# Kernel optimization log

Hardware: AMD Instinct MI355X
Metric: run time of the kernel (lower is better)

The kernel has to match this reference:

```python
import jax, jax.numpy as jnp
import numpy as np

B, N, C = 4, 2048, 768
H = 12
HD = C // H

def setup_inputs() -> dict:
    key = jax.random.key(0)
    k1, k2, k3, k4, k5 = jax.random.split(key, 5)
    x = jax.random.normal(k1, (B, N, C), dtype=jnp.float32)
    qkv_w = jax.random.normal(k2, (3 * C, C), dtype=jnp.float32) * (1.0 / np.sqrt(C))
    qkv_b = jax.random.normal(k3, (3 * C,), dtype=jnp.float32) * 0.02
    proj_w = jax.random.normal(k4, (C, C), dtype=jnp.float32) * (1.0 / np.sqrt(C))
    proj_b = jax.random.normal(k5, (C,), dtype=jnp.float32) * 0.02
    return {"x": x, "qkv_w": qkv_w, "qkv_b": qkv_b, "proj_w": proj_w, "proj_b": proj_b}

def reference(x, qkv_w, qkv_b, proj_w, proj_b):
    scale = HD ** (-0.5)
    # qkv projection: (B,N,3C)
    qkv = x @ qkv_w.T + qkv_b
    qkv = qkv.reshape(B, N, 3, H, HD).transpose(2, 0, 3, 1, 4)  # (3,B,H,N,HD)
    q, k, v = qkv[0], qkv[1], qkv[2]
    attn = jnp.einsum('bhqd,bhkd->bhqk', q, k) * scale  # (B,H,N,N)
    mask_value = -jnp.finfo(attn.dtype).max
    causal_mask = jnp.triu(jnp.ones((N, N), dtype=bool), k=1)
    attn = jnp.where(causal_mask, mask_value, attn)
    attn = jax.nn.softmax(attn, axis=-1)
    out = jnp.einsum('bhqk,bhkd->bhqd', attn, v)  # (B,H,N,HD)
    out = out.transpose(0, 2, 1, 3).reshape(B, N, C)
    return out @ proj_w.T + proj_b
```

## Files before the change

kernel.cpp:

```cpp
#include <hip/hip_runtime.h>
#include <hip/hip_bf16.h>


typedef __attribute__((ext_vector_type(8))) short bf16x8;
typedef __attribute__((ext_vector_type(4))) float f32x4;
typedef __attribute__((ext_vector_type(16))) float f32x16;

typedef __attribute__((address_space(3))) unsigned int lds_uint;
typedef __attribute__((address_space(1))) const unsigned int gbl_uint;

__device__ __forceinline__ void gload16(const void* g, void* l) {
  __builtin_amdgcn_global_load_lds((gbl_uint*)g, (lds_uint*)l, 16, 0, 0);
}

__device__ __forceinline__ unsigned short f2bf(float f) {
  unsigned u = __float_as_uint(f);
  unsigned rounding = 0x7FFFu + ((u >> 16) & 1u);
  return (unsigned short)((u + rounding) >> 16);
}

__device__ __forceinline__ unsigned cvtpk(float lo, float hi) {
  unsigned r;
  asm("v_cvt_pk_bf16_f32 %0, %1, %2" : "=v"(r) : "v"(lo), "v"(hi));
  return r;
}

__device__ __forceinline__ float exp2a(float x) {
  float r;
  asm("v_exp_f32 %0, %1" : "=v"(r) : "v"(x));
  return r;
}

__global__ void cast_f32_to_bf16(const float* __restrict__ in,
                                 unsigned short* __restrict__ out, int n) {
  int idx = blockIdx.x * blockDim.x + threadIdx.x;
  int stride = gridDim.x * blockDim.x;
  for (int i = idx * 4; i < n; i += stride * 4) {
    float4 v = *reinterpret_cast<const float4*>(in + i);
    ushort4 o;
    o.x = f2bf(v.x); o.y = f2bf(v.y); o.z = f2bf(v.z); o.w = f2bf(v.w);
    *reinterpret_cast<ushort4*>(out + i) = o;
  }
}

template <bool OUT_F32>
__global__ __launch_bounds__(256) void gemm_bt_kernel(
    const unsigned short* __restrict__ A,
    const unsigned short* __restrict__ Bw,
    const float* __restrict__ bias,
    void* __restrict__ Cout,
    int M, int Ncols, int K, int ldc) {
  __shared__ __align__(16) short As[2][4096];
  __shared__ __align__(16) short Bs[2][4096];

  const int t = threadIdx.x;
  const int lane = t & 63;
  const int wave = t >> 6;
  const int wm = wave >> 1;
  const int wn = wave & 1;
  const int m0 = blockIdx.y * 128;
  const int n0 = blockIdx.x * 128;
  const int lrow = lane & 15;
  const int lk = (lane >> 4) * 8;

  const int srow = t >> 2, scol = (t & 3) * 8;
  const unsigned short* gA0 = A + (size_t)(m0 + srow) * K + scol;
  const unsigned short* gA1 = gA0 + (size_t)64 * K;
  const unsigned short* gB0 = Bw + (size_t)(n0 + srow) * K + scol;
  const unsigned short* gB1 = gB0 + (size_t)64 * K;
  const int db0 = wave * 512, db1 = 2048 + wave * 512;

  f32x4 acc[4][4] = {};
  const int nk = K / 32;

  gload16(gA0, &As[0][db0]); gload16(gA1, &As[0][db1]);
  gload16(gB0, &Bs[0][db0]); gload16(gB1, &Bs[0][db1]);

  int cur = 0;
  for (int kk = 0; kk < nk; ++kk) {
    __syncthreads();
    if (kk + 1 < nk) {
      const int off = (kk + 1) * 32;
      gload16(gA0 + off, &As[cur ^ 1][db0]); gload16(gA1 + off, &As[cur ^ 1][db1]);
      gload16(gB0 + off, &Bs[cur ^ 1][db0]); gload16(gB1 + off, &Bs[cur ^ 1][db1]);
    }
    bf16x8 a[4], b[4];
#pragma unroll
    for (int m = 0; m < 4; ++m)
      a[m] = *reinterpret_cast<const bf16x8*>(&As[cur][(wm * 64 + m * 16 + lrow) * 32 + lk]);
#pragma unroll
    for (int n = 0; n < 4; ++n)
      b[n] = *reinterpret_cast<const bf16x8*>(&Bs[cur][(wn * 64 + n * 16 + lrow) * 32 + lk]);
#pragma unroll
    for (int m = 0; m < 4; ++m)
#pragma unroll
      for (int n = 0; n < 4; ++n)
        acc[m][n] = __builtin_amdgcn_mfma_f32_16x16x32_bf16(a[m], b[n], acc[m][n], 0, 0, 0);
    cur ^= 1;
  }

  const int orow0 = (lane >> 4) * 4;
  const int ocol = lane & 15;
#pragma unroll
  for (int m = 0; m < 4; ++m) {
#pragma unroll
    for (int n = 0; n < 4; ++n) {
      const int c = n0 + wn * 64 + n * 16 + ocol;
      const float bv = bias[c];
#pragma unroll
      for (int r = 0; r < 4; ++r) {
        const int rr = m0 + wm * 64 + m * 16 + orow0 + r;
        const float v = acc[m][n][r] + bv;
        if (OUT_F32)
          reinterpret_cast<float*>(Cout)[(size_t)rr * ldc + c] = v;
        else
          reinterpret_cast<unsigned short*>(Cout)[(size_t)rr * ldc + c] = f2bf(v);
      }
    }
  }
}

#define ATT_N 2048
#define ATT_H 12
#define QKV_LD 2304

__global__ __launch_bounds__(256) void transpose_v(
    const unsigned short* __restrict__ qkv, unsigned short* __restrict__ vt) {
  __shared__ __align__(16) short L[128 * 72];
  const int kb = blockIdx.x;
  const int bh = blockIdx.y;
  const int t = threadIdx.x;
  const int b = bh / ATT_H, h = bh % ATT_H;
  const int d0 = (t & 7) * 8;
  const int kl0 = t >> 3;
  const unsigned short* src =
      qkv + (size_t)(b * ATT_N + kb * 128) * QKV_LD + 1536 + h * 64 + d0;
#pragma unroll
  for (int r = 0; r < 4; ++r) {
    const int kl = kl0 + r * 32;
    bf16x8 v = *reinterpret_cast<const bf16x8*>(src + (size_t)kl * QKV_LD);
    *reinterpret_cast<bf16x8*>(&L[kl * 72 + d0]) = v;
  }
  __syncthreads();
  const int d = t >> 2;
  const int c = t & 3;
  unsigned short* dst = vt + (size_t)bh * 64 * ATT_N + (size_t)d * ATT_N + kb * 128;
#pragma unroll
  for (int cc = 0; cc < 4; ++cc) {
    const int kc = cc * 32 + c * 8;
    union { unsigned short s[8]; bf16x8 v; } U;
#pragma unroll
    for (int j = 0; j < 8; ++j) U.s[j] = (unsigned short)L[(kc + j) * 72 + d];
    *reinterpret_cast<bf16x8*>(dst + kc) = U.v;
  }
}

__global__ __launch_bounds__(256) void attn_kernel(
    const unsigned short* __restrict__ qkv,
    const unsigned short* __restrict__ vt,
    unsigned short* __restrict__ out) {
  __shared__ __align__(16) short Ks[2][4096];
  __shared__ __align__(16) short Vs[2][4096];

  const int t = threadIdx.x;
  const int lane = t & 63;
  const int w = t >> 6;
  const int hi = lane >> 5;
  const int l31 = lane & 31;

  const int wid = blockIdx.x;
  const int qb = 15 - (wid / 48);
  const int bh = wid % 48;
  const int b = bh / ATT_H;
  const int h = bh % ATT_H;

  const size_t rowbase = (size_t)b * ATT_N;
  const unsigned short* qptr = qkv + rowbase * QKV_LD + h * 64;
  const unsigned short* kptr = qptr + 768;
  const unsigned short* vtptr = vt + (size_t)bh * 64 * ATT_N;

  const int q0w = qb * 128 + w * 32;
  const int qg = q0w + l31;
  const int nt = (qb + 1) * 2;

  bf16x8 qf[4];
#pragma unroll
  for (int dk = 0; dk < 4; ++dk)
    qf[dk] = *reinterpret_cast<const bf16x8*>(
        qptr + (size_t)(q0w + l31) * QKV_LD + dk * 16 + hi * 8);

  f32x16 O0 = {}, O1 = {};
  float lrun = 0.f;

  int kKr[2], kKc[2];
#pragma unroll
  for (int c = 0; c < 2; ++c) {
    const int i = t + c * 256;
    const int f = i >> 6, ls = i & 63;
    kKr[c] = (f >> 2) * 32 + (ls & 31);
    kKc[c] = (f & 3) * 2 + (ls >> 5);
  }
  const unsigned short* gK0 = kptr + (size_t)kKr[0] * QKV_LD + kKc[0] * 8;
  const unsigned short* gK1 = kptr + (size_t)kKr[1] * QKV_LD + kKc[1] * 8;
  const unsigned short* gV0 = vtptr + (size_t)kKr[0] * ATT_N + kKc[0] * 8;
  const unsigned short* gV1 = vtptr + (size_t)kKr[1] * ATT_N + kKc[1] * 8;
  const int db0 = w * 512, db1 = 2048 + w * 512;

  gload16(gK0, &Ks[0][db0]); gload16(gK1, &Ks[0][db1]);
  gload16(gV0, &Vs[0][db0]); gload16(gV1, &Vs[0][db1]);

  int cur = 0;
  for (int kt = 0; kt < nt; ++kt) {
    const int k0 = kt * 64;
    __syncthreads();
    if (kt + 1 < nt) {
      const size_t advk = (size_t)(k0 + 64) * QKV_LD;
      gload16(gK0 + advk, &Ks[cur ^ 1][db0]); gload16(gK1 + advk, &Ks[cur ^ 1][db1]);
      gload16(gV0 + (k0 + 64), &Vs[cur ^ 1][db0]);
      gload16(gV1 + (k0 + 64), &Vs[cur ^ 1][db1]);
    }

    if (k0 <= q0w + 31) {
      f32x16 S0 = {}, S1 = {};
      __builtin_amdgcn_s_setprio(1);
#pragma unroll
      for (int dk = 0; dk < 4; ++dk) {
        bf16x8 kf = *reinterpret_cast<const bf16x8*>(&Ks[cur][(dk * 64 + lane) * 8]);
        S0 = __builtin_amdgcn_mfma_f32_32x32x16_bf16(kf, qf[dk], S0, 0, 0, 0);
      }
#pragma unroll
      for (int dk = 0; dk < 4; ++dk) {
        bf16x8 kf = *reinterpret_cast<const bf16x8*>(&Ks[cur][((4 + dk) * 64 + lane) * 8]);
        S1 = __builtin_amdgcn_mfma_f32_32x32x16_bf16(kf, qf[dk], S1, 0, 0, 0);
      }
      __builtin_amdgcn_s_setprio(0);

      const float scale2 = 0.18033688f;
      float p0[16], p1[16];
      if (k0 + 63 <= q0w) {
#pragma unroll
        for (int r = 0; r < 16; ++r) {
          p0[r] = exp2a(S0[r] * scale2);
          p1[r] = exp2a(S1[r] * scale2);
        }
      } else {
#pragma unroll
        for (int r = 0; r < 16; ++r) {
          int row = (r & 3) + 8 * (r >> 2) + 4 * hi;
          float e0 = (k0 + row > qg) ? -1e30f : S0[r] * scale2;
          float e1 = (k0 + 32 + row > qg) ? -1e30f : S1[r] * scale2;
          p0[r] = exp2a(e0);
          p1[r] = exp2a(e1);
        }
      }

      float sa = 0.f, sb = 0.f;
#pragma unroll
      for (int r = 0; r < 16; r += 2) { sa += p0[r] + p1[r]; sb += p0[r + 1] + p1[r + 1]; }
      float rsum = sa + sb;
      rsum += __shfl_xor(rsum, 32);
      lrun += rsum;

      bf16x8 Ub[4];
#pragma unroll
      for (int s = 0; s < 2; ++s) {
        unsigned pu[4][2];
#pragma unroll
        for (int m = 0; m < 4; ++m)
#pragma unroll
          for (int c = 0; c < 2; ++c)
            pu[m][c] = s ? cvtpk(p1[4 * m + 2 * c], p1[4 * m + 2 * c + 1])
                         : cvtpk(p0[4 * m + 2 * c], p0[4 * m + 2 * c + 1]);
#pragma unroll
        for (int tt = 0; tt < 2; ++tt) {
          unsigned s0v = hi ? pu[2 * tt][0] : pu[2 * tt + 1][0];
          unsigned s1v = hi ? pu[2 * tt][1] : pu[2 * tt + 1][1];
          unsigned r0 = __shfl_xor(s0v, 32);
          unsigned r1 = __shfl_xor(s1v, 32);
          union { unsigned u[4]; bf16x8 v; } U;
          U.u[0] = hi ? r0 : pu[2 * tt][0];
          U.u[1] = hi ? r1 : pu[2 * tt][1];
          U.u[2] = hi ? pu[2 * tt + 1][0] : r0;
          U.u[3] = hi ? pu[2 * tt + 1][1] : r1;
          Ub[s * 2 + tt] = U.v;
        }
      }

      __builtin_amdgcn_s_setprio(1);
#pragma unroll
      for (int ks = 0; ks < 4; ++ks) {
        bf16x8 vf0 = *reinterpret_cast<const bf16x8*>(&Vs[cur][(ks * 64 + lane) * 8]);
        O0 = __builtin_amdgcn_mfma_f32_32x32x16_bf16(vf0, Ub[ks], O0, 0, 0, 0);
        bf16x8 vf1 = *reinterpret_cast<const bf16x8*>(&Vs[cur][((4 + ks) * 64 + lane) * 8]);
        O1 = __builtin_amdgcn_mfma_f32_32x32x16_bf16(vf1, Ub[ks], O1, 0, 0, 0);
      }
      __builtin_amdgcn_s_setprio(0);
    }
    cur ^= 1;
  }

  const float inv = 1.0f / lrun;
  unsigned short* orow = out + (rowbase + q0w + l31) * 768 + h * 64;
#pragma unroll
  for (int half = 0; half < 2; ++half) {
    const f32x16& O = half ? O1 : O0;
#pragma unroll
    for (int m = 0; m < 4; ++m) {
      uint2 o2;
      o2.x = cvtpk(O[4 * m + 0] * inv, O[4 * m + 1] * inv);
      o2.y = cvtpk(O[4 * m + 2] * inv, O[4 * m + 3] * inv);
      *reinterpret_cast<uint2*>(orow + half * 32 + 8 * m + 4 * hi) = o2;
    }
  }
}

extern "C" void kernel_launch(void* const* d_in, const int* in_sizes, int n_in,
                              void* d_out, int out_size, void* d_ws, size_t ws_size,
                              hipStream_t stream) {
  const float* x = (const float*)d_in[0];
  const float* qkv_w = (const float*)d_in[1];
  const float* qkv_b = (const float*)d_in[2];
  const float* proj_w = (const float*)d_in[3];
  const float* proj_b = (const float*)d_in[4];
  float* out = (float*)d_out;

  unsigned short* x_bf = (unsigned short*)d_ws;
  unsigned short* qw_bf = x_bf + (size_t)8192 * 768;
  unsigned short* pw_bf = qw_bf + (size_t)2304 * 768;
  unsigned short* qkv = pw_bf + (size_t)768 * 768;
  unsigned short* attno = qkv + (size_t)8192 * 2304;
  unsigned short* vtb = attno + (size_t)8192 * 768;

  cast_f32_to_bf16<<<dim3(1024), dim3(256), 0, stream>>>(x, x_bf, 8192 * 768);
  cast_f32_to_bf16<<<dim3(512), dim3(256), 0, stream>>>(qkv_w, qw_bf, 2304 * 768);
  cast_f32_to_bf16<<<dim3(256), dim3(256), 0, stream>>>(proj_w, pw_bf, 768 * 768);

  gemm_bt_kernel<false><<<dim3(18, 64), dim3(256), 0, stream>>>(
      x_bf, qw_bf, qkv_b, qkv, 8192, 2304, 768, 2304);
  transpose_v<<<dim3(16, 48), dim3(256), 0, stream>>>(qkv, vtb);
  attn_kernel<<<dim3(768), dim3(256), 0, stream>>>(qkv, vtb, attno);
  gemm_bt_kernel<true><<<dim3(6, 64), dim3(256), 0, stream>>>(
      attno, pw_bf, proj_b, out, 8192, 768, 768, 768);
}
```

Before: 150.4 us.

## Restructure attention into single-wave blocks with 32-key tiles and no barriers

```diff
diff --git a/kernel.cpp b/kernel.cpp
--- a/kernel.cpp
+++ b/kernel.cpp
@@ -155,21 +155,19 @@
   }
 }
 
-__global__ __launch_bounds__(256) void attn_kernel(
+__global__ __launch_bounds__(64) void attn_kernel(
     const unsigned short* __restrict__ qkv,
     const unsigned short* __restrict__ vt,
     unsigned short* __restrict__ out) {
-  __shared__ __align__(16) short Ks[2][4096];
-  __shared__ __align__(16) short Vs[2][4096];
-
-  const int t = threadIdx.x;
-  const int lane = t & 63;
-  const int w = t >> 6;
+  __shared__ __align__(16) short Ks[2][2048];
+  __shared__ __align__(16) short Vs[2][2048];
+
+  const int lane = threadIdx.x;
   const int hi = lane >> 5;
   const int l31 = lane & 31;
 
   const int wid = blockIdx.x;
-  const int qb = 15 - (wid / 48);
+  const int qc = 63 - (wid / 48);
   const int bh = wid % 48;
   const int b = bh / ATT_H;
   const int h = bh % ATT_H;
@@ -179,9 +177,9 @@
   const unsigned short* kptr = qptr + 768;
   const unsigned short* vtptr = vt + (size_t)bh * 64 * ATT_N;
 
-  const int q0w = qb * 128 + w * 32;
+  const int q0w = qc * 32;
   const int qg = q0w + l31;
-  const int nt = (qb + 1) * 2;
+  const int nt = qc + 1;
 
   bf16x8 qf[4];
 #pragma unroll
@@ -192,110 +190,89 @@
   f32x16 O0 = {}, O1 = {};
   float lrun = 0.f;
 
-  int kKr[2], kKc[2];
-#pragma unroll
-  for (int c = 0; c < 2; ++c) {
-    const int i = t + c * 256;
-    const int f = i >> 6, ls = i & 63;
-    kKr[c] = (f >> 2) * 32 + (ls & 31);
-    kKc[c] = (f & 3) * 2 + (ls >> 5);
-  }
-  const unsigned short* gK0 = kptr + (size_t)kKr[0] * QKV_LD + kKc[0] * 8;
-  const unsigned short* gK1 = kptr + (size_t)kKr[1] * QKV_LD + kKc[1] * 8;
-  const unsigned short* gV0 = vtptr + (size_t)kKr[0] * ATT_N + kKc[0] * 8;
-  const unsigned short* gV1 = vtptr + (size_t)kKr[1] * ATT_N + kKc[1] * 8;
-  const int db0 = w * 512, db1 = 2048 + w * 512;
-
-  gload16(gK0, &Ks[0][db0]); gload16(gK1, &Ks[0][db1]);
-  gload16(gV0, &Vs[0][db0]); gload16(gV1, &Vs[0][db1]);
+  auto stage = [&](int k0, int buf) {
+    const unsigned short* kr = kptr + (size_t)(k0 + l31) * QKV_LD + hi * 8;
+#pragma unroll
+    for (int g = 0; g < 4; ++g)
+      gload16(kr + g * 16, &Ks[buf][g * 512]);
+    const unsigned short* vr = vtptr + (size_t)l31 * ATT_N + k0 + hi * 8;
+#pragma unroll
+    for (int g = 0; g < 4; ++g)
+      gload16(vr + (size_t)(g >> 1) * 32 * ATT_N + (g & 1) * 16, &Vs[buf][g * 512]);
+  };
+
+  stage(0, 0);
 
   int cur = 0;
   for (int kt = 0; kt < nt; ++kt) {
-    const int k0 = kt * 64;
-    __syncthreads();
+    const int k0 = kt * 32;
     if (kt + 1 < nt) {
-      const size_t advk = (size_t)(k0 + 64) * QKV_LD;
-      gload16(gK0 + advk, &Ks[cur ^ 1][db0]); gload16(gK1 + advk, &Ks[cur ^ 1][db1]);
-      gload16(gV0 + (k0 + 64), &Vs[cur ^ 1][db0]);
-      gload16(gV1 + (k0 + 64), &Vs[cur ^ 1][db1]);
-    }
-
-    if (k0 <= q0w + 31) {
-      f32x16 S0 = {}, S1 = {};
-      __builtin_amdgcn_s_setprio(1);
-#pragma unroll
-      for (int dk = 0; dk < 4; ++dk) {
-        bf16x8 kf = *reinterpret_cast<const bf16x8*>(&Ks[cur][(dk * 64 + lane) * 8]);
-        S0 = __builtin_amdgcn_mfma_f32_32x32x16_bf16(kf, qf[dk], S0, 0, 0, 0);
+      stage(k0 + 32, cur ^ 1);
+      asm volatile("s_waitcnt vmcnt(8)" ::: "memory");
+    } else {
+      asm volatile("s_waitcnt vmcnt(0)" ::: "memory");
+    }
+
+    f32x16 S0 = {};
+    __builtin_amdgcn_s_setprio(1);
+#pragma unroll
+    for (int dk = 0; dk < 4; ++dk) {
+      bf16x8 kf = *reinterpret_cast<const bf16x8*>(&Ks[cur][(dk * 64 + lane) * 8]);
+      S0 = __builtin_amdgcn_mfma_f32_32x32x16_bf16(kf, qf[dk], S0, 0, 0, 0);
+    }
+    __builtin_amdgcn_s_setprio(0);
+
+    const float scale2 = 0.18033688f;
+    float p0[16];
+    if (k0 + 31 <= q0w) {
+#pragma unroll
+      for (int r = 0; r < 16; ++r) p0[r] = exp2a(S0[r] * scale2);
+    } else {
+#pragma unroll
+      for (int r = 0; r < 16; ++r) {
+        const int key = k0 + (r & 3) + 8 * (r >> 2) + 4 * hi;
+        p0[r] = exp2a((key > qg) ? -1e30f : S0[r] * scale2);
       }
-#pragma unroll
-      for (int dk = 0; dk < 4; ++dk) {
-        bf16x8 kf = *reinterpret_cast<const bf16x8*>(&Ks[cur][((4 + dk) * 64 + lane) * 8]);
-        S1 = __builtin_amdgcn_mfma_f32_32x32x16_bf16(kf, qf[dk], S1, 0, 0, 0);
-      }
-      __builtin_amdgcn_s_setprio(0);
-
-      const float scale2 = 0.18033688f;
-      float p0[16], p1[16];
-      if (k0 + 63 <= q0w) {
-#pragma unroll
-        for (int r = 0; r < 16; ++r) {
-          p0[r] = exp2a(S0[r] * scale2);
-          p1[r] = exp2a(S1[r] * scale2);
-        }
-      } else {
-#pragma unroll
-        for (int r = 0; r < 16; ++r) {
-          int row = (r & 3) + 8 * (r >> 2) + 4 * hi;
-          float e0 = (k0 + row > qg) ? -1e30f : S0[r] * scale2;
-          float e1 = (k0 + 32 + row > qg) ? -1e30f : S1[r] * scale2;
-          p0[r] = exp2a(e0);
-          p1[r] = exp2a(e1);
-        }
-      }
-
-      float sa = 0.f, sb = 0.f;
-#pragma unroll
-      for (int r = 0; r < 16; r += 2) { sa += p0[r] + p1[r]; sb += p0[r + 1] + p1[r + 1]; }
-      float rsum = sa + sb;
-      rsum += __shfl_xor(rsum, 32);
-      lrun += rsum;
-
-      bf16x8 Ub[4];
-#pragma unroll
-      for (int s = 0; s < 2; ++s) {
-        unsigned pu[4][2];
-#pragma unroll
-        for (int m = 0; m < 4; ++m)
-#pragma unroll
-          for (int c = 0; c < 2; ++c)
-            pu[m][c] = s ? cvtpk(p1[4 * m + 2 * c], p1[4 * m + 2 * c + 1])
-                         : cvtpk(p0[4 * m + 2 * c], p0[4 * m + 2 * c + 1]);
-#pragma unroll
-        for (int tt = 0; tt < 2; ++tt) {
-          unsigned s0v = hi ? pu[2 * tt][0] : pu[2 * tt + 1][0];
-          unsigned s1v = hi ? pu[2 * tt][1] : pu[2 * tt + 1][1];
-          unsigned r0 = __shfl_xor(s0v, 32);
-          unsigned r1 = __shfl_xor(s1v, 32);
-          union { unsigned u[4]; bf16x8 v; } U;
-          U.u[0] = hi ? r0 : pu[2 * tt][0];
-          U.u[1] = hi ? r1 : pu[2 * tt][1];
-          U.u[2] = hi ? pu[2 * tt + 1][0] : r0;
-          U.u[3] = hi ? pu[2 * tt + 1][1] : r1;
-          Ub[s * 2 + tt] = U.v;
-        }
-      }
-
-      __builtin_amdgcn_s_setprio(1);
-#pragma unroll
-      for (int ks = 0; ks < 4; ++ks) {
-        bf16x8 vf0 = *reinterpret_cast<const bf16x8*>(&Vs[cur][(ks * 64 + lane) * 8]);
-        O0 = __builtin_amdgcn_mfma_f32_32x32x16_bf16(vf0, Ub[ks], O0, 0, 0, 0);
-        bf16x8 vf1 = *reinterpret_cast<const bf16x8*>(&Vs[cur][((4 + ks) * 64 + lane) * 8]);
-        O1 = __builtin_amdgcn_mfma_f32_32x32x16_bf16(vf1, Ub[ks], O1, 0, 0, 0);
-      }
-      __builtin_amdgcn_s_setprio(0);
-    }
+    }
+
+    float sa = 0.f, sb = 0.f;
+#pragma unroll
+    for (int r = 0; r < 16; r += 2) { sa += p0[r]; sb += p0[r + 1]; }
+    float rsum = sa + sb;
+    rsum += __shfl_xor(rsum, 32);
+    lrun += rsum;
+
+    unsigned pu[4][2];
+#pragma unroll
+    for (int m = 0; m < 4; ++m)
+#pragma unroll
+      for (int c = 0; c < 2; ++c)
+        pu[m][c] = cvtpk(p0[4 * m + 2 * c], p0[4 * m + 2 * c + 1]);
+    bf16x8 Ub[2];
+#pragma unroll
+    for (int tt = 0; tt < 2; ++tt) {
+      unsigned s0v = hi ? pu[2 * tt][0] : pu[2 * tt + 1][0];
+      unsigned s1v = hi ? pu[2 * tt][1] : pu[2 * tt + 1][1];
+      unsigned r0 = __shfl_xor(s0v, 32);
+      unsigned r1 = __shfl_xor(s1v, 32);
+      union { unsigned u[4]; bf16x8 v; } U;
+      U.u[0] = hi ? r0 : pu[2 * tt][0];
+      U.u[1] = hi ? r1 : pu[2 * tt][1];
+      U.u[2] = hi ? pu[2 * tt + 1][0] : r0;
+      U.u[3] = hi ? pu[2 * tt + 1][1] : r1;
+      Ub[tt] = U.v;
+    }
+
+    __builtin_amdgcn_s_setprio(1);
+#pragma unroll
+    for (int tt = 0; tt < 2; ++tt) {
+      bf16x8 vf0 = *reinterpret_cast<const bf16x8*>(&Vs[cur][(tt * 64 + lane) * 8]);
+      O0 = __builtin_amdgcn_mfma_f32_32x32x16_bf16(vf0, Ub[tt], O0, 0, 0, 0);
+      bf16x8 vf1 = *reinterpret_cast<const bf16x8*>(&Vs[cur][((2 + tt) * 64 + lane) * 8]);
+      O1 = __builtin_amdgcn_mfma_f32_32x32x16_bf16(vf1, Ub[tt], O1, 0, 0, 0);
+    }
+    __builtin_amdgcn_s_setprio(0);
+
     cur ^= 1;
   }
 
@@ -338,7 +315,7 @@
   gemm_bt_kernel<false><<<dim3(18, 64), dim3(256), 0, stream>>>(
       x_bf, qw_bf, qkv_b, qkv, 8192, 2304, 768, 2304);
   transpose_v<<<dim3(16, 48), dim3(256), 0, stream>>>(qkv, vtb);
-  attn_kernel<<<dim3(768), dim3(256), 0, stream>>>(qkv, vtb, attno);
+  attn_kernel<<<dim3(3072), dim3(64), 0, stream>>>(qkv, vtb, attno);
   gemm_bt_kernel<true><<<dim3(6, 64), dim3(256), 0, stream>>>(
       attno, pw_bf, proj_b, out, 8192, 768, 768, 768);
 }
```

Result: slower. 194.7 us (+29.5%).

## Make attention kernel persistent with atomic work-queue scheduling

Applied to the files above, without the earlier changes.

```diff
diff --git a/kernel.cpp b/kernel.cpp
--- a/kernel.cpp
+++ b/kernel.cpp
@@ -158,7 +158,8 @@
 __global__ __launch_bounds__(256) void attn_kernel(
     const unsigned short* __restrict__ qkv,
     const unsigned short* __restrict__ vt,
-    unsigned short* __restrict__ out) {
+    unsigned short* __restrict__ out,
+    int* __restrict__ ctr) {
   __shared__ __align__(16) short Ks[2][4096];
   __shared__ __align__(16) short Vs[2][4096];
 
@@ -168,30 +169,6 @@
   const int hi = lane >> 5;
   const int l31 = lane & 31;
 
-  const int wid = blockIdx.x;
-  const int qb = 15 - (wid / 48);
-  const int bh = wid % 48;
-  const int b = bh / ATT_H;
-  const int h = bh % ATT_H;
-
-  const size_t rowbase = (size_t)b * ATT_N;
-  const unsigned short* qptr = qkv + rowbase * QKV_LD + h * 64;
-  const unsigned short* kptr = qptr + 768;
-  const unsigned short* vtptr = vt + (size_t)bh * 64 * ATT_N;
-
-  const int q0w = qb * 128 + w * 32;
-  const int qg = q0w + l31;
-  const int nt = (qb + 1) * 2;
-
-  bf16x8 qf[4];
-#pragma unroll
-  for (int dk = 0; dk < 4; ++dk)
-    qf[dk] = *reinterpret_cast<const bf16x8*>(
-        qptr + (size_t)(q0w + l31) * QKV_LD + dk * 16 + hi * 8);
-
-  f32x16 O0 = {}, O1 = {};
-  float lrun = 0.f;
-
   int kKr[2], kKc[2];
 #pragma unroll
   for (int c = 0; c < 2; ++c) {
@@ -200,116 +177,149 @@
     kKr[c] = (f >> 2) * 32 + (ls & 31);
     kKc[c] = (f & 3) * 2 + (ls >> 5);
   }
-  const unsigned short* gK0 = kptr + (size_t)kKr[0] * QKV_LD + kKc[0] * 8;
-  const unsigned short* gK1 = kptr + (size_t)kKr[1] * QKV_LD + kKc[1] * 8;
-  const unsigned short* gV0 = vtptr + (size_t)kKr[0] * ATT_N + kKc[0] * 8;
-  const unsigned short* gV1 = vtptr + (size_t)kKr[1] * ATT_N + kKc[1] * 8;
   const int db0 = w * 512, db1 = 2048 + w * 512;
 
-  gload16(gK0, &Ks[0][db0]); gload16(gK1, &Ks[0][db1]);
-  gload16(gV0, &Vs[0][db0]); gload16(gV1, &Vs[0][db1]);
-
-  int cur = 0;
-  for (int kt = 0; kt < nt; ++kt) {
-    const int k0 = kt * 64;
+  for (;;) {
     __syncthreads();
-    if (kt + 1 < nt) {
-      const size_t advk = (size_t)(k0 + 64) * QKV_LD;
-      gload16(gK0 + advk, &Ks[cur ^ 1][db0]); gload16(gK1 + advk, &Ks[cur ^ 1][db1]);
-      gload16(gV0 + (k0 + 64), &Vs[cur ^ 1][db0]);
-      gload16(gV1 + (k0 + 64), &Vs[cur ^ 1][db1]);
+    if (t == 0) *reinterpret_cast<int*>(&Ks[0][0]) = atomicAdd(ctr, 1);
+    __syncthreads();
+    const int u = *reinterpret_cast<const int*>(&Ks[0][0]);
+    if (u >= 768) break;
+    __syncthreads();
+
+    const int qb = 15 - (u / 48);
+    const int bh = u % 48;
+    const int b = bh / ATT_H;
+    const int h = bh % ATT_H;
+
+    const size_t rowbase = (size_t)b * ATT_N;
+    const unsigned short* qptr = qkv + rowbase * QKV_LD + h * 64;
+    const unsigned short* kptr = qptr + 768;
+    const unsigned short* vtptr = vt + (size_t)bh * 64 * ATT_N;
+
+    const int q0w = qb * 128 + w * 32;
+    const int qg = q0w + l31;
+    const int nt = (qb + 1) * 2;
+
+    bf16x8 qf[4];
+#pragma unroll
+    for (int dk = 0; dk < 4; ++dk)
+      qf[dk] = *reinterpret_cast<const bf16x8*>(
+          qptr + (size_t)(q0w + l31) * QKV_LD + dk * 16 + hi * 8);
+
+    f32x16 O0 = {}, O1 = {};
+    float lrun = 0.f;
+
+    const unsigned short* gK0 = kptr + (size_t)kKr[0] * QKV_LD + kKc[0] * 8;
+    const unsigned short* gK1 = kptr + (size_t)kKr[1] * QKV_LD + kKc[1] * 8;
+    const unsigned short* gV0 = vtptr + (size_t)kKr[0] * ATT_N + kKc[0] * 8;
+    const unsigned short* gV1 = vtptr + (size_t)kKr[1] * ATT_N + kKc[1] * 8;
+
+    gload16(gK0, &Ks[0][db0]); gload16(gK1, &Ks[0][db1]);
+    gload16(gV0, &Vs[0][db0]); gload16(gV1, &Vs[0][db1]);
+
+    int cur = 0;
+    for (int kt = 0; kt < nt; ++kt) {
+      const int k0 = kt * 64;
+      __syncthreads();
+      if (kt + 1 < nt) {
+        const size_t advk = (size_t)(k0 + 64) * QKV_LD;
+        gload16(gK0 + advk, &Ks[cur ^ 1][db0]); gload16(gK1 + advk, &Ks[cur ^ 1][db1]);
+        gload16(gV0 + (k0 + 64), &Vs[cur ^ 1][db0]);
+        gload16(gV1 + (k0 + 64), &Vs[cur ^ 1][db1]);
+      }
+
+      if (k0 <= q0w + 31) {
+        f32x16 S0 = {}, S1 = {};
+        __builtin_amdgcn_s_setprio(1);
+#pragma unroll
+        for (int dk = 0; dk < 4; ++dk) {
+          bf16x8 kf = *reinterpret_cast<const bf16x8*>(&Ks[cur][(dk * 64 + lane) * 8]);
+          S0 = __builtin_amdgcn_mfma_f32_32x32x16_bf16(kf, qf[dk], S0, 0, 0, 0);
+        }
+#pragma unroll
+        for (int dk = 0; dk < 4; ++dk) {
+          bf16x8 kf = *reinterpret_cast<const bf16x8*>(&Ks[cur][((4 + dk) * 64 + lane) * 8]);
+          S1 = __builtin_amdgcn_mfma_f32_32x32x16_bf16(kf, qf[dk], S1, 0, 0, 0);
+        }
+        __builtin_amdgcn_s_setprio(0);
+
+        const float scale2 = 0.18033688f;
+        float p0[16], p1[16];
+        if (k0 + 63 <= q0w) {
+#pragma unroll
+          for (int r = 0; r < 16; ++r) {
+            p0[r] = exp2a(S0[r] * scale2);
+            p1[r] = exp2a(S1[r] * scale2);
+          }
+        } else {
+#pragma unroll
+          for (int r = 0; r < 16; ++r) {
+            int row = (r & 3) + 8 * (r >> 2) + 4 * hi;
+            float e0 = (k0 + row > qg) ? -1e30f : S0[r] * scale2;
+            float e1 = (k0 + 32 + row > qg) ? -1e30f : S1[r] * scale2;
+            p0[r] = exp2a(e0);
+            p1[r] = exp2a(e1);
+          }
+        }
+
+        float sa = 0.f, sb = 0.f;
+#pragma unroll
+        for (int r = 0; r < 16; r += 2) { sa += p0[r] + p1[r]; sb += p0[r + 1] + p1[r + 1]; }
+        float rsum = sa + sb;
+        rsum += __shfl_xor(rsum, 32);
+        lrun += rsum;
+
+        bf16x8 Ub[4];
+#pragma unroll
+        for (int s = 0; s < 2; ++s) {
+          unsigned pu[4][2];
+#pragma unroll
+          for (int m = 0; m < 4; ++m)
+#pragma unroll
+            for (int c = 0; c < 2; ++c)
+              pu[m][c] = s ? cvtpk(p1[4 * m + 2 * c], p1[4 * m + 2 * c + 1])
+                           : cvtpk(p0[4 * m + 2 * c], p0[4 * m + 2 * c + 1]);
+#pragma unroll
+          for (int tt = 0; tt < 2; ++tt) {
+            unsigned s0v = hi ? pu[2 * tt][0] : pu[2 * tt + 1][0];
+            unsigned s1v = hi ? pu[2 * tt][1] : pu[2 * tt + 1][1];
+            unsigned r0 = __shfl_xor(s0v, 32);
+            unsigned r1 = __shfl_xor(s1v, 32);
+            union { unsigned uu[4]; bf16x8 v; } U;
+            U.uu[0] = hi ? r0 : pu[2 * tt][0];
+            U.uu[1] = hi ? r1 : pu[2 * tt][1];
+            U.uu[2] = hi ? pu[2 * tt + 1][0] : r0;
+            U.uu[3] = hi ? pu[2 * tt + 1][1] : r1;
+            Ub[s * 2 + tt] = U.v;
+          }
+        }
+
+        __builtin_amdgcn_s_setprio(1);
+#pragma unroll
+        for (int ks = 0; ks < 4; ++ks) {
+          bf16x8 vf0 = *reinterpret_cast<const bf16x8*>(&Vs[cur][(ks * 64 + lane) * 8]);
+          O0 = __builtin_amdgcn_mfma_f32_32x32x16_bf16(vf0, Ub[ks], O0, 0, 0, 0);
+          bf16x8 vf1 = *reinterpret_cast<const bf16x8*>(&Vs[cur][((4 + ks) * 64 + lane) * 8]);
+          O1 = __builtin_amdgcn_mfma_f32_32x32x16_bf16(vf1, Ub[ks], O1, 0, 0, 0);
+        }
+        __builtin_amdgcn_s_setprio(0);
+      }
+      cur ^= 1;
     }
 
-    if (k0 <= q0w + 31) {
-      f32x16 S0 = {}, S1 = {};
-      __builtin_amdgcn_s_setprio(1);
-#pragma unroll
-      for (int dk = 0; dk < 4; ++dk) {
-        bf16x8 kf = *reinterpret_cast<const bf16x8*>(&Ks[cur][(dk * 64 + lane) * 8]);
-        S0 = __builtin_amdgcn_mfma_f32_32x32x16_bf16(kf, qf[dk], S0, 0, 0, 0);
+    const float inv = 1.0f / lrun;
+    unsigned short* orow = out + (rowbase + q0w + l31) * 768 + h * 64;
+#pragma unroll
+    for (int half = 0; half < 2; ++half) {
+      const f32x16& O = half ? O1 : O0;
+#pragma unroll
+      for (int m = 0; m < 4; ++m) {
+        uint2 o2;
+        o2.x = cvtpk(O[4 * m + 0] * inv, O[4 * m + 1] * inv);
+        o2.y = cvtpk(O[4 * m + 2] * inv, O[4 * m + 3] * inv);
+        *reinterpret_cast<uint2*>(orow + half * 32 + 8 * m + 4 * hi) = o2;
       }
-#pragma unroll
-      for (int dk = 0; dk < 4; ++dk) {
-        bf16x8 kf = *reinterpret_cast<const bf16x8*>(&Ks[cur][((4 + dk) * 64 + lane) * 8]);
-        S1 = __builtin_amdgcn_mfma_f32_32x32x16_bf16(kf, qf[dk], S1, 0, 0, 0);
-      }
-      __builtin_amdgcn_s_setprio(0);
-
-      const float scale2 = 0.18033688f;
-      float p0[16], p1[16];
-      if (k0 + 63 <= q0w) {
-#pragma unroll
-        for (int r = 0; r < 16; ++r) {
-          p0[r] = exp2a(S0[r] * scale2);
-          p1[r] = exp2a(S1[r] * scale2);
-        }
-      } else {
-#pragma unroll
-        for (int r = 0; r < 16; ++r) {
-          int row = (r & 3) + 8 * (r >> 2) + 4 * hi;
-          float e0 = (k0 + row > qg) ? -1e30f : S0[r] * scale2;
-          float e1 = (k0 + 32 + row > qg) ? -1e30f : S1[r] * scale2;
-          p0[r] = exp2a(e0);
-          p1[r] = exp2a(e1);
-        }
-      }
-
-      float sa = 0.f, sb = 0.f;
-#pragma unroll
-      for (int r = 0; r < 16; r += 2) { sa += p0[r] + p1[r]; sb += p0[r + 1] + p1[r + 1]; }
-      float rsum = sa + sb;
-      rsum += __shfl_xor(rsum, 32);
-      lrun += rsum;
-
-      bf16x8 Ub[4];
-#pragma unroll
-      for (int s = 0; s < 2; ++s) {
-        unsigned pu[4][2];
-#pragma unroll
-        for (int m = 0; m < 4; ++m)
-#pragma unroll
-          for (int c = 0; c < 2; ++c)
-            pu[m][c] = s ? cvtpk(p1[4 * m + 2 * c], p1[4 * m + 2 * c + 1])
-                         : cvtpk(p0[4 * m + 2 * c], p0[4 * m + 2 * c + 1]);
-#pragma unroll
-        for (int tt = 0; tt < 2; ++tt) {
-          unsigned s0v = hi ? pu[2 * tt][0] : pu[2 * tt + 1][0];
-          unsigned s1v = hi ? pu[2 * tt][1] : pu[2 * tt + 1][1];
-          unsigned r0 = __shfl_xor(s0v, 32);
-          unsigned r1 = __shfl_xor(s1v, 32);
-          union { unsigned u[4]; bf16x8 v; } U;
-          U.u[0] = hi ? r0 : pu[2 * tt][0];
-          U.u[1] = hi ? r1 : pu[2 * tt][1];
-          U.u[2] = hi ? pu[2 * tt + 1][0] : r0;
-          U.u[3] = hi ? pu[2 * tt + 1][1] : r1;
-          Ub[s * 2 + tt] = U.v;
-        }
-      }
-
-      __builtin_amdgcn_s_setprio(1);
-#pragma unroll
-      for (int ks = 0; ks < 4; ++ks) {
-        bf16x8 vf0 = *reinterpret_cast<const bf16x8*>(&Vs[cur][(ks * 64 + lane) * 8]);
-        O0 = __builtin_amdgcn_mfma_f32_32x32x16_bf16(vf0, Ub[ks], O0, 0, 0, 0);
-        bf16x8 vf1 = *reinterpret_cast<const bf16x8*>(&Vs[cur][((4 + ks) * 64 + lane) * 8]);
-        O1 = __builtin_amdgcn_mfma_f32_32x32x16_bf16(vf1, Ub[ks], O1, 0, 0, 0);
-      }
-      __builtin_amdgcn_s_setprio(0);
-    }
-    cur ^= 1;
-  }
-
-  const float inv = 1.0f / lrun;
-  unsigned short* orow = out + (rowbase + q0w + l31) * 768 + h * 64;
-#pragma unroll
-  for (int half = 0; half < 2; ++half) {
-    const f32x16& O = half ? O1 : O0;
-#pragma unroll
-    for (int m = 0; m < 4; ++m) {
-      uint2 o2;
-      o2.x = cvtpk(O[4 * m + 0] * inv, O[4 * m + 1] * inv);
-      o2.y = cvtpk(O[4 * m + 2] * inv, O[4 * m + 3] * inv);
-      *reinterpret_cast<uint2*>(orow + half * 32 + 8 * m + 4 * hi) = o2;
     }
   }
 }
@@ -330,15 +340,17 @@
   unsigned short* qkv = pw_bf + (size_t)768 * 768;
   unsigned short* attno = qkv + (size_t)8192 * 2304;
   unsigned short* vtb = attno + (size_t)8192 * 768;
+  int* ctr = (int*)(vtb + (size_t)48 * 64 * 2048);
 
   cast_f32_to_bf16<<<dim3(1024), dim3(256), 0, stream>>>(x, x_bf, 8192 * 768);
   cast_f32_to_bf16<<<dim3(512), dim3(256), 0, stream>>>(qkv_w, qw_bf, 2304 * 768);
   cast_f32_to_bf16<<<dim3(256), dim3(256), 0, stream>>>(proj_w, pw_bf, 768 * 768);
+  hipMemsetAsync(ctr, 0, sizeof(int), stream);
 
   gemm_bt_kernel<false><<<dim3(18, 64), dim3(256), 0, stream>>>(
       x_bf, qw_bf, qkv_b, qkv, 8192, 2304, 768, 2304);
   transpose_v<<<dim3(16, 48), dim3(256), 0, stream>>>(qkv, vtb);
-  attn_kernel<<<dim3(768), dim3(256), 0, stream>>>(qkv, vtb, attno);
+  attn_kernel<<<dim3(1280), dim3(256), 0, stream>>>(qkv, vtb, attno, ctr);
   gemm_bt_kernel<true><<<dim3(6, 64), dim3(256), 0, stream>>>(
       attno, pw_bf, proj_b, out, 8192, 768, 768, 768);
 }
```

New measurement: 161.7 us. 1.08x slower.
